# Kernel optimization log

Measured on AMD Instinct MI355X. Metric: run time of the kernel, lower is better.

## Reference

```python
import jax, jax.numpy as jnp
import numpy as np

D_MODEL = 1024
H = 16
D_K = D_MODEL // H
B = 4
S = 2048


def setup_inputs() -> dict:
    key = jax.random.key(0)
    ks = jax.random.split(key, 7)
    q = jax.random.normal(ks[0], (B, S, D_MODEL), dtype=jnp.float32)
    k = jax.random.normal(ks[1], (B, S, D_MODEL), dtype=jnp.float32)
    v = jax.random.normal(ks[2], (B, S, D_MODEL), dtype=jnp.float32)
    # nn.Linear weights have shape (out_features, in_features); y = x @ W.T
    scale = 1.0 / np.sqrt(D_MODEL)
    w_q = jax.random.normal(ks[3], (D_MODEL, D_MODEL), dtype=jnp.float32) * scale
    w_k = jax.random.normal(ks[4], (D_MODEL, D_MODEL), dtype=jnp.float32) * scale
    w_v = jax.random.normal(ks[5], (D_MODEL, D_MODEL), dtype=jnp.float32) * scale
    w_o = jax.random.normal(ks[6], (D_MODEL, D_MODEL), dtype=jnp.float32) * scale
    mask = jnp.ones((1, 1, S, S), dtype=bool)  # broadcasts over [B,H,S,S]
    return {"q": q, "k": k, "v": v, "w_q": w_q, "w_k": w_k, "w_v": w_v,
            "w_o": w_o, "mask": mask}


def reference(q, k, v, w_q, w_k, w_v, w_o, mask):
    # projections (nn.Linear, no bias): x @ W.T
    query = jnp.einsum('bsd,ed->bse', q, w_q)
    key_p = jnp.einsum('bsd,ed->bse', k, w_k)
    value = jnp.einsum('bsd,ed->bse', v, w_v)
    # split heads: [B,S,D] -> [B,H,S,d_k]
    query = query.reshape(B, S, H, D_K).transpose(0, 2, 1, 3)
    key_p = key_p.reshape(B, S, H, D_K).transpose(0, 2, 1, 3)
    value = value.reshape(B, S, H, D_K).transpose(0, 2, 1, 3)
    # scaled dot-product attention (explicit softmax, as in source)
    scores = jnp.einsum('bhqd,bhkd->bhqk', query, key_p) / jnp.sqrt(
        jnp.asarray(D_K, dtype=query.dtype))
    scores = jnp.where(mask, scores, jnp.asarray(-1e9, dtype=scores.dtype))
    weights = jax.nn.softmax(scores, axis=-1)
    ctx = jnp.einsum('bhqk,bhkd->bhqd', weights, value)
    # merge heads and output projection
    ctx = ctx.transpose(0, 2, 1, 3).reshape(B, S, D_MODEL)
    return jnp.einsum('bsd,ed->bse', ctx, w_o)
```

## Files before the change

kernel.cpp:

```cpp
#include <hip/hip_runtime.h>
#include <hip/hip_bf16.h>
#include <stdint.h>
#include <math.h>

#define DM 1024
#define SS 2048
#define HH 16

typedef unsigned short u16;
typedef __attribute__((ext_vector_type(8))) short short8;
typedef __attribute__((ext_vector_type(4))) float f32x4;
typedef __attribute__((ext_vector_type(4))) unsigned short u16x4;

#define C_SCALE 0.18033688011112042f

__device__ __forceinline__ u16 f2bf(float f) {
    union { float f; uint32_t u; } v; v.f = f;
    uint32_t r = v.u + 0x7FFFu + ((v.u >> 16) & 1u);
    return (u16)(r >> 16);
}

__device__ __forceinline__ void async_cp16(const void* g, void* l) {
    __builtin_amdgcn_global_load_lds(
        reinterpret_cast<const __attribute__((address_space(1))) unsigned int*>(
            reinterpret_cast<uintptr_t>(g)),
        reinterpret_cast<__attribute__((address_space(3))) unsigned int*>(
            reinterpret_cast<uintptr_t>(l)),
        16, 0, 0);
}

__global__ __launch_bounds__(256) void cast_bf16(const float* __restrict__ in,
                                                 u16* __restrict__ out, int n4)
{
    int i = blockIdx.x * 256 + threadIdx.x;
    if (i < n4) {
        float4 v = ((const float4*)in)[i];
        u16x4 p = { f2bf(v.x), f2bf(v.y), f2bf(v.z), f2bf(v.w) };
        ((u16x4*)out)[i] = p;
    }
}

__global__ __launch_bounds__(256) void cast_w4(const float* __restrict__ w0,
                                               const float* __restrict__ w1,
                                               const float* __restrict__ w2,
                                               const float* __restrict__ w3,
                                               u16* __restrict__ o0,
                                               u16* __restrict__ o1,
                                               u16* __restrict__ o2,
                                               u16* __restrict__ o3)
{
    const uint32_t which = blockIdx.x >> 10;
    const uint32_t i = (blockIdx.x & 1023u) * 256u + threadIdx.x;
    const float* in = which == 0 ? w0 : which == 1 ? w1 : which == 2 ? w2 : w3;
    u16* out = which == 0 ? o0 : which == 1 ? o1 : which == 2 ? o2 : o3;
    float4 v = ((const float4*)in)[i];
    u16x4 p = { f2bf(v.x), f2bf(v.y), f2bf(v.z), f2bf(v.w) };
    ((u16x4*)out)[i] = p;
}

template<int MODE>
__global__ __launch_bounds__(256) void gemm_bt(const u16* __restrict__ A,
                                               const u16* __restrict__ B,
                                               void* __restrict__ C)
{
    __shared__ char sm[32768];
    const uint32_t t = threadIdx.x;
    const uint32_t l = t & 63u, w = t >> 6;
    uint32_t id = blockIdx.x;
    id = (id & 7u) * 64u + (id >> 3);
    const uint32_t bm = id >> 3, bn = id & 7u;
    const uint32_t wr = w >> 1, wc = w & 1u;

    const uint32_t q15 = l & 15u, G = l >> 4, xq = q15 & 7u;
    const uint32_t vbg0 = q15 * 128u + ((G ^ (xq & 3u)) << 4) + ((xq >> 2) << 6);
    const uint32_t vA0 = wr * 8192u + vbg0,          vA1 = vA0 ^ 64u;
    const uint32_t vB0 = 16384u + wc * 8192u + vbg0, vB1 = vB0 ^ 64u;

    uint32_t La[4];
    const u16* aP[4];
    const u16* bP[4];
    #pragma unroll
    for (uint32_t i = 0; i < 4; ++i) {
        La[i] = (i * 256u + t) * 16u;
        const uint32_t r = La[i] >> 7;
        const uint32_t c8 = ((La[i] >> 4) & 7u) ^ (r & 7u);
        aP[i] = A + (size_t)(bm * 128u + r) * DM + c8 * 8u;
        bP[i] = B + (size_t)(bn * 128u + r) * DM + c8 * 8u;
    }

    f32x4 acc[4][4] = {};

    for (uint32_t k0 = 0; k0 < 1024; k0 += 64) {
        __syncthreads();
        #pragma unroll
        for (uint32_t i = 0; i < 4; ++i) async_cp16(aP[i] + k0, sm + La[i]);
        #pragma unroll
        for (uint32_t i = 0; i < 4; ++i) async_cp16(bP[i] + k0, sm + 16384 + La[i]);
        __syncthreads();

        #pragma unroll
        for (uint32_t kk = 0; kk < 2; ++kk) {
            const uint32_t va = kk ? vA1 : vA0;
            const uint32_t vb = kk ? vB1 : vB0;
            short8 a[4], b[4];
            #pragma unroll
            for (uint32_t m = 0; m < 4; ++m)
                a[m] = *(const short8*)(sm + va + m * 2048u);
            #pragma unroll
            for (uint32_t n = 0; n < 4; ++n)
                b[n] = *(const short8*)(sm + vb + n * 2048u);
            #pragma unroll
            for (uint32_t m = 0; m < 4; ++m)
                #pragma unroll
                for (uint32_t n = 0; n < 4; ++n)
                    acc[m][n] = __builtin_amdgcn_mfma_f32_16x16x32_bf16(
                        a[m], b[n], acc[m][n], 0, 0, 0);
        }
    }

    #pragma unroll
    for (uint32_t m = 0; m < 4; ++m) {
        #pragma unroll
        for (uint32_t n = 0; n < 4; ++n) {
            const uint32_t rmb = bm * 128u + wr * 64u + m * 16u + G * 4u;
            const uint32_t cn  = bn * 128u + wc * 64u + n * 16u + q15;
            if (MODE == 0 || MODE == 3) {
                const float sc = (MODE == 3) ? C_SCALE : 1.0f;
                #pragma unroll
                for (uint32_t g = 0; g < 4; ++g)
                    ((u16*)C)[(size_t)(rmb + g) * DM + cn] = f2bf(acc[m][n][g] * sc);
            } else if (MODE == 1) {
                const uint32_t b_ = rmb >> 11, s0 = rmb & 2047u;
                u16x4 pk;
                #pragma unroll
                for (uint32_t g = 0; g < 4; ++g) pk[g] = f2bf(acc[m][n][g]);
                *(u16x4*)((u16*)C + (size_t)(b_ * 1024u + cn) * 2048u + s0) = pk;
            } else {
                #pragma unroll
                for (uint32_t g = 0; g < 4; ++g)
                    ((float*)C)[(size_t)(rmb + g) * DM + cn] = acc[m][n][g];
            }
        }
    }
}

__global__ __launch_bounds__(512) void attn_mfma(const u16* __restrict__ Q,
                                                 const u16* __restrict__ K,
                                                 const u16* __restrict__ Vt,
                                                 u16* __restrict__ ctx)
{
    __shared__ char sm[69632];
    const uint32_t t = threadIdx.x, l = t & 63u, w = t >> 6;
    uint32_t id = blockIdx.x;
    id = (id & 7u) * 64u + (id >> 3);
    const uint32_t qt = id & 7u, h = (id >> 3) & 15u, b = id >> 7;

    const uint32_t q15 = l & 15u, G = l >> 4, xq = q15 & 7u;

    const uint32_t vb0 = q15 * 128u + ((G ^ (xq & 3u)) << 4) + ((xq >> 2) << 6);
    const uint32_t vb1 = vb0 ^ 64u;
    const uint32_t vbPw = w * 4608u + q15 * 144u + G * 8u;
    const uint32_t vbPr = w * 4608u + q15 * 144u + G * 16u;

    short8 qf[2][2];
    #pragma unroll
    for (uint32_t qb = 0; qb < 2; ++qb) {
        const size_t qrow = (size_t)(b * 2048u + qt * 256u + w * 32u + qb * 16u + q15);
        const uint32_t col = h * 64u + (G << 3);
        qf[qb][0] = *(const short8*)(Q + qrow * DM + col);
        qf[qb][1] = *(const short8*)(Q + qrow * DM + col + 32u);
    }

    short8 ones;
    #pragma unroll
    for (int i = 0; i < 8; ++i) ones[i] = (short)0x3F80;
    const f32x4 ZV = {0.f, 0.f, 0.f, 0.f};

    f32x4 o[2][4] = {};
    f32x4 osum[2] = {};

    const uint32_t Ls = t * 16u;
    const u16* kcur;
    const u16* vcur;
    {
        const size_t kbase = (size_t)b * 2048u * DM + h * 64u;
        const size_t vbase = (size_t)((b * 16u + h) * 64u) * 2048u;
        const uint32_t r = Ls >> 7;
        const uint32_t c8 = ((Ls >> 4) & 7u) ^ (r & 7u);
        const u16* k0p = K  + kbase + (size_t)r * DM    + c8 * 8u;
        const u16* v0p = Vt + vbase + (size_t)r * 2048u + c8 * 8u;
        async_cp16(k0p, sm + Ls);
        async_cp16(v0p, sm + 8192 + Ls);
        kcur = k0p + (size_t)64u * DM;
        vcur = v0p + 64u;
    }

#define ATTN_STEP(BCc, BNc, STAGE)                                             \
    {                                                                          \
        if (STAGE) {                                                           \
            async_cp16(kcur, sm + (BNc) + Ls);                                 \
            async_cp16(vcur, sm + (BNc) + 8192u + Ls);                         \
            kcur += (size_t)64u * DM;                                          \
            vcur += 64u;                                                       \
            asm volatile("s_waitcnt vmcnt(2)" ::: "memory");                   \
        } else {                                                               \
            asm volatile("s_waitcnt vmcnt(0)" ::: "memory");                   \
        }                                                                      \
        __builtin_amdgcn_s_barrier();                                          \
        __builtin_amdgcn_sched_barrier(0);                                     \
        f32x4 s[2][4];                                                         \
        __builtin_amdgcn_s_setprio(1);                                         \
        _Pragma("unroll")                                                      \
        for (uint32_t mf = 0; mf < 4; ++mf) {                                  \
            short8 kf0 = *(const short8*)(sm + (BCc) + vb0 + mf * 2048u);      \
            short8 kf1 = *(const short8*)(sm + (BCc) + vb1 + mf * 2048u);      \
            _Pragma("unroll")                                                  \
            for (uint32_t qb = 0; qb < 2; ++qb) {                              \
                s[qb][mf] = __builtin_amdgcn_mfma_f32_16x16x32_bf16(           \
                    kf1, qf[qb][1],                                            \
                    __builtin_amdgcn_mfma_f32_16x16x32_bf16(                   \
                        kf0, qf[qb][0], ZV, 0, 0, 0),                          \
                    0, 0, 0);                                                  \
            }                                                                  \
        }                                                                      \
        __builtin_amdgcn_s_setprio(0);                                         \
        _Pragma("unroll")                                                      \
        for (uint32_t qb = 0; qb < 2; ++qb) {                                  \
            _Pragma("unroll")                                                  \
            for (uint32_t mf = 0; mf < 4; ++mf) {                              \
                float p0 = __builtin_amdgcn_exp2f(s[qb][mf][0]);               \
                float p1 = __builtin_amdgcn_exp2f(s[qb][mf][1]);               \
                float p2 = __builtin_amdgcn_exp2f(s[qb][mf][2]);               \
                float p3 = __builtin_amdgcn_exp2f(s[qb][mf][3]);               \
                union { u16x4 v; struct { __hip_bfloat162 lo, hi; } b; } pk;   \
                pk.b.lo = __float22bfloat162_rn(make_float2(p0, p1));          \
                pk.b.hi = __float22bfloat162_rn(make_float2(p2, p3));          \
                *(u16x4*)(sm + 32768u + vbPw + qb * 2304u + mf * 32u) = pk.v;  \
            }                                                                  \
        }                                                                      \
        _Pragma("unroll")                                                      \
        for (uint32_t kk = 0; kk < 2; ++kk) {                                  \
            const uint32_t vv = (kk ? vb1 : vb0) + 8192u;                      \
            short8 vf[4];                                                      \
            _Pragma("unroll")                                                  \
            for (uint32_t d = 0; d < 4; ++d)                                   \
                vf[d] = *(const short8*)(sm + (BCc) + vv + d * 2048u);         \
            __builtin_amdgcn_s_setprio(1);                                     \
            _Pragma("unroll")                                                  \
            for (uint32_t qb = 0; qb < 2; ++qb) {                              \
                short8 pf = *(const short8*)(sm + 32768u + vbPr +              \
                                             qb * 2304u + kk * 64u);           \
                _Pragma("unroll")                                              \
                for (uint32_t d = 0; d < 4; ++d)                               \
                    o[qb][d] = __builtin_amdgcn_mfma_f32_16x16x32_bf16(        \
                        pf, vf[d], o[qb][d], 0, 0, 0);                         \
                osum[qb] = __builtin_amdgcn_mfma_f32_16x16x32_bf16(            \
                    pf, ones, osum[qb], 0, 0, 0);                              \
            }                                                                  \
            __builtin_amdgcn_s_setprio(0);                                     \
        }                                                                      \
        asm volatile("s_waitcnt lgkmcnt(0)" ::: "memory");                     \
        __builtin_amdgcn_s_barrier();                                          \
        __builtin_amdgcn_sched_barrier(0);                                     \
    }

    for (uint32_t it = 0; it < 15; ++it) {
        ATTN_STEP(0u, 16384u, true)
        ATTN_STEP(16384u, 0u, true)
    }
    ATTN_STEP(0u, 16384u, true)
    ATTN_STEP(16384u, 0u, false)

#undef ATTN_STEP

    #pragma unroll
    for (uint32_t qb = 0; qb < 2; ++qb) {
        float inv[4];
        #pragma unroll
        for (int g = 0; g < 4; ++g) inv[g] = 1.0f / osum[qb][g];
        #pragma unroll
        for (uint32_t d = 0; d < 4; ++d)
            #pragma unroll
            for (int g = 0; g < 4; ++g) {
                const uint32_t srow = qt * 256u + w * 32u + qb * 16u + G * 4u + (uint32_t)g;
                const uint32_t col  = h * 64u + d * 16u + q15;
                ctx[(size_t)(b * 2048u + srow) * DM + col] = f2bf(o[qb][d][g] * inv[g]);
            }
    }
}

extern "C" void kernel_launch(void* const* d_in, const int* in_sizes, int n_in,
                              void* d_out, int out_size, void* d_ws, size_t ws_size,
                              hipStream_t stream)
{
    const float* q  = (const float*)d_in[0];
    const float* k  = (const float*)d_in[1];
    const float* v  = (const float*)d_in[2];
    const float* wq = (const float*)d_in[3];
    const float* wk = (const float*)d_in[4];
    const float* wv = (const float*)d_in[5];
    const float* wo = (const float*)d_in[6];

    const size_t SZ = (size_t)4 * 2048 * 1024;
    const size_t WZ = (size_t)1024 * 1024;
    u16* qb  = (u16*)d_ws;
    u16* Qp  = qb  + SZ;
    u16* Kp  = Qp  + SZ;
    u16* Vtp = Kp  + SZ;
    u16* wqb = Vtp + SZ;
    u16* wkb = wqb + WZ;
    u16* wvb = wkb + WZ;
    u16* wob = wvb + WZ;

    cast_w4<<<4096, 256, 0, stream>>>(wq, wk, wv, wo, wqb, wkb, wvb, wob);

    cast_bf16<<<8192, 256, 0, stream>>>(q, qb, (int)(SZ / 4));
    gemm_bt<3><<<512, 256, 0, stream>>>(qb, wqb, Qp);
    cast_bf16<<<8192, 256, 0, stream>>>(k, qb, (int)(SZ / 4));
    gemm_bt<0><<<512, 256, 0, stream>>>(qb, wkb, Kp);
    cast_bf16<<<8192, 256, 0, stream>>>(v, qb, (int)(SZ / 4));
    gemm_bt<1><<<512, 256, 0, stream>>>(qb, wvb, Vtp);

    attn_mfma<<<512, 512, 0, stream>>>(Qp, Kp, Vtp, qb);

    gemm_bt<2><<<512, 256, 0, stream>>>(qb, wob, d_out);
}
```

Baseline: 194.7 us.

## Fuse input fp32-to-bf16 cast into a single batched QKV projection GEMM

Removes the three standalone cast kernels by loading fp32 activations directly in the projection GEMM, converting them to bf16 in registers and storing them into LDS. The Q, K and V projections are merged into one 1536-block launch that selects operands and epilogue per block. This avoids writing and re-reading bf16 copies of the inputs and cuts launch count, in exchange for a register-staged A path with higher register use and more global read bytes per tile.

```diff
diff --git a/kernel.cpp b/kernel.cpp
--- a/kernel.cpp
+++ b/kernel.cpp
@@ -29,15 +29,13 @@
         16, 0, 0);
 }
 
-__global__ __launch_bounds__(256) void cast_bf16(const float* __restrict__ in,
-                                                 u16* __restrict__ out, int n4)
-{
-    int i = blockIdx.x * 256 + threadIdx.x;
-    if (i < n4) {
-        float4 v = ((const float4*)in)[i];
-        u16x4 p = { f2bf(v.x), f2bf(v.y), f2bf(v.z), f2bf(v.w) };
-        ((u16x4*)out)[i] = p;
-    }
+__device__ __forceinline__ short8 pack8(const float4 a, const float4 b) {
+    union { short8 s; struct { __hip_bfloat162 p0, p1, p2, p3; } p; } u;
+    u.p.p0 = __float22bfloat162_rn(make_float2(a.x, a.y));
+    u.p.p1 = __float22bfloat162_rn(make_float2(a.z, a.w));
+    u.p.p2 = __float22bfloat162_rn(make_float2(b.x, b.y));
+    u.p.p3 = __float22bfloat162_rn(make_float2(b.z, b.w));
+    return u.s;
 }
 
 __global__ __launch_bounds__(256) void cast_w4(const float* __restrict__ w0,
@@ -58,10 +56,125 @@
     ((u16x4*)out)[i] = p;
 }
 
-template<int MODE>
-__global__ __launch_bounds__(256) void gemm_bt(const u16* __restrict__ A,
-                                               const u16* __restrict__ B,
-                                               void* __restrict__ C)
+__global__ __launch_bounds__(256) void gemm_proj(const float* __restrict__ Aq,
+                                                 const float* __restrict__ Ak,
+                                                 const float* __restrict__ Av,
+                                                 const u16* __restrict__ Bq,
+                                                 const u16* __restrict__ Bk,
+                                                 const u16* __restrict__ Bv,
+                                                 u16* __restrict__ Cq,
+                                                 u16* __restrict__ Ck,
+                                                 u16* __restrict__ Cv)
+{
+    __shared__ char sm[32768];
+    const uint32_t t = threadIdx.x;
+    const uint32_t l = t & 63u, w = t >> 6;
+    const uint32_t sw = (blockIdx.x & 7u) * 192u + (blockIdx.x >> 3);
+    const uint32_t which = sw >> 9;
+    const uint32_t inner = sw & 511u;
+    const uint32_t bm = inner >> 3, bn = inner & 7u;
+    const uint32_t wr = w >> 1, wc = w & 1u;
+
+    const float* A = which == 0 ? Aq : which == 1 ? Ak : Av;
+    const u16*   B = which == 0 ? Bq : which == 1 ? Bk : Bv;
+
+    const uint32_t q15 = l & 15u, G = l >> 4, xq = q15 & 7u;
+    const uint32_t vbg0 = q15 * 128u + ((G ^ (xq & 3u)) << 4) + ((xq >> 2) << 6);
+    const uint32_t vA0 = wr * 8192u + vbg0,          vA1 = vA0 ^ 64u;
+    const uint32_t vB0 = 16384u + wc * 8192u + vbg0, vB1 = vB0 ^ 64u;
+
+    const float* aP[4];
+    uint32_t aD[4];
+    #pragma unroll
+    for (uint32_t i = 0; i < 4; ++i) {
+        const uint32_t j = i * 256u + t, row = j >> 3, cc = j & 7u;
+        aP[i] = A + (size_t)(bm * 128u + row) * DM + cc * 8u;
+        aD[i] = row * 128u + ((cc ^ (row & 7u)) << 4);
+    }
+    uint32_t La[4];
+    const u16* bP[4];
+    #pragma unroll
+    for (uint32_t i = 0; i < 4; ++i) {
+        La[i] = (i * 256u + t) * 16u;
+        const uint32_t r = La[i] >> 7;
+        const uint32_t c8 = ((La[i] >> 4) & 7u) ^ (r & 7u);
+        bP[i] = B + (size_t)(bn * 128u + r) * DM + c8 * 8u;
+    }
+
+    f32x4 acc[4][4] = {};
+    float4 av[4][2];
+    #pragma unroll
+    for (uint32_t i = 0; i < 4; ++i) {
+        av[i][0] = *(const float4*)(aP[i]);
+        av[i][1] = *(const float4*)(aP[i] + 4);
+    }
+
+    for (uint32_t k0 = 0; k0 < 1024; k0 += 64) {
+        __syncthreads();
+        #pragma unroll
+        for (uint32_t i = 0; i < 4; ++i)
+            *(short8*)(sm + aD[i]) = pack8(av[i][0], av[i][1]);
+        #pragma unroll
+        for (uint32_t i = 0; i < 4; ++i) async_cp16(bP[i] + k0, sm + 16384 + La[i]);
+        __syncthreads();
+
+        if (k0 != 960u) {
+            #pragma unroll
+            for (uint32_t i = 0; i < 4; ++i) {
+                av[i][0] = *(const float4*)(aP[i] + k0 + 64u);
+                av[i][1] = *(const float4*)(aP[i] + k0 + 68u);
+            }
+        }
+
+        #pragma unroll
+        for (uint32_t kk = 0; kk < 2; ++kk) {
+            const uint32_t va = kk ? vA1 : vA0;
+            const uint32_t vb = kk ? vB1 : vB0;
+            short8 a[4], b[4];
+            #pragma unroll
+            for (uint32_t m = 0; m < 4; ++m)
+                a[m] = *(const short8*)(sm + va + m * 2048u);
+            #pragma unroll
+            for (uint32_t n = 0; n < 4; ++n)
+                b[n] = *(const short8*)(sm + vb + n * 2048u);
+            #pragma unroll
+            for (uint32_t m = 0; m < 4; ++m)
+                #pragma unroll
+                for (uint32_t n = 0; n < 4; ++n)
+                    acc[m][n] = __builtin_amdgcn_mfma_f32_16x16x32_bf16(
+                        a[m], b[n], acc[m][n], 0, 0, 0);
+        }
+    }
+
+    u16* Cb = which == 0 ? Cq : which == 1 ? Ck : Cv;
+    #pragma unroll
+    for (uint32_t m = 0; m < 4; ++m) {
+        #pragma unroll
+        for (uint32_t n = 0; n < 4; ++n) {
+            const uint32_t rmb = bm * 128u + wr * 64u + m * 16u + G * 4u;
+            const uint32_t cn  = bn * 128u + wc * 64u + n * 16u + q15;
+            if (which == 0) {
+                #pragma unroll
+                for (uint32_t g = 0; g < 4; ++g)
+                    Cb[(size_t)(rmb + g) * DM + cn] = f2bf(acc[m][n][g] * C_SCALE);
+            } else if (which == 1) {
+                #pragma unroll
+                for (uint32_t g = 0; g < 4; ++g)
+                    Cb[(size_t)(rmb + g) * DM + cn] = f2bf(acc[m][n][g]);
+            } else {
+                const uint32_t b_ = rmb >> 11, s0 = rmb & 2047u;
+                u16x4 pk;
+                #pragma unroll
+                for (uint32_t g = 0; g < 4; ++g) pk[g] = f2bf(acc[m][n][g]);
+                *(u16x4*)(Cb + (size_t)(b_ * 1024u + cn) * 2048u + s0) = pk;
+            }
+        }
+    }
+}
+
+__global__ __launch_bounds__(256) void gemm_out(const u16* __restrict__ A,
+                                                const u16* __restrict__ B,
+                                                float* __restrict__ C)
 {
     __shared__ char sm[32768];
     const uint32_t t = threadIdx.x;
@@ -124,22 +237,9 @@
         for (uint32_t n = 0; n < 4; ++n) {
             const uint32_t rmb = bm * 128u + wr * 64u + m * 16u + G * 4u;
             const uint32_t cn  = bn * 128u + wc * 64u + n * 16u + q15;
-            if (MODE == 0 || MODE == 3) {
-                const float sc = (MODE == 3) ? C_SCALE : 1.0f;
-                #pragma unroll
-                for (uint32_t g = 0; g < 4; ++g)
-                    ((u16*)C)[(size_t)(rmb + g) * DM + cn] = f2bf(acc[m][n][g] * sc);
-            } else if (MODE == 1) {
-                const uint32_t b_ = rmb >> 11, s0 = rmb & 2047u;
-                u16x4 pk;
-                #pragma unroll
-                for (uint32_t g = 0; g < 4; ++g) pk[g] = f2bf(acc[m][n][g]);
-                *(u16x4*)((u16*)C + (size_t)(b_ * 1024u + cn) * 2048u + s0) = pk;
-            } else {
-                #pragma unroll
-                for (uint32_t g = 0; g < 4; ++g)
-                    ((float*)C)[(size_t)(rmb + g) * DM + cn] = acc[m][n][g];
-            }
+            #pragma unroll
+            for (uint32_t g = 0; g < 4; ++g)
+                C[(size_t)(rmb + g) * DM + cn] = acc[m][n][g];
         }
     }
 }
@@ -303,8 +403,8 @@
 
     const size_t SZ = (size_t)4 * 2048 * 1024;
     const size_t WZ = (size_t)1024 * 1024;
-    u16* qb  = (u16*)d_ws;
-    u16* Qp  = qb  + SZ;
+    u16* ctx = (u16*)d_ws;
+    u16* Qp  = ctx + SZ;
     u16* Kp  = Qp  + SZ;
     u16* Vtp = Kp  + SZ;
     u16* wqb = Vtp + SZ;
@@ -314,14 +414,9 @@
 
     cast_w4<<<4096, 256, 0, stream>>>(wq, wk, wv, wo, wqb, wkb, wvb, wob);
 
-    cast_bf16<<<8192, 256, 0, stream>>>(q, qb, (int)(SZ / 4));
-    gemm_bt<3><<<512, 256, 0, stream>>>(qb, wqb, Qp);
-    cast_bf16<<<8192, 256, 0, stream>>>(k, qb, (int)(SZ / 4));
-    gemm_bt<0><<<512, 256, 0, stream>>>(qb, wkb, Kp);
-    cast_bf16<<<8192, 256, 0, stream>>>(v, qb, (int)(SZ / 4));
-    gemm_bt<1><<<512, 256, 0, stream>>>(qb, wvb, Vtp);
-
-    attn_mfma<<<512, 512, 0, stream>>>(Qp, Kp, Vtp, qb);
-
-    gemm_bt<2><<<512, 256, 0, stream>>>(qb, wob, d_out);
-}
+    gemm_proj<<<1536, 256, 0, stream>>>(q, k, v, wqb, wkb, wvb, Qp, Kp, Vtp);
+
+    attn_mfma<<<512, 512, 0, stream>>>(Qp, Kp, Vtp, ctx);
+
+    gemm_out<<<512, 256, 0, stream>>>(ctx, wob, (float*)d_out);
+}
```

Result: slower. 217.0 us (+11.5%).
